# Kernel tuning notes

Measured on AMD Instinct MI355X. Metric: run time of the kernel, lower is better.

Reference implementation:

```python
import jax, jax.numpy as jnp
import numpy as np

B, T, C = 4, 2048, 1024
HEAD = 64  # n_embd // n_heads


def setup_inputs() -> dict:
    key = jax.random.key(0)
    kx, kk, kq, kv = jax.random.split(key, 4)
    x = jax.random.normal(kx, (B, T, C), dtype=jnp.float32)
    # nn.Linear(n_embd, head_size, bias=False) weights have shape [head_size, n_embd]
    s = 1.0 / np.sqrt(C)
    Wk = jax.random.normal(kk, (HEAD, C), dtype=jnp.float32) * s
    Wq = jax.random.normal(kq, (HEAD, C), dtype=jnp.float32) * s
    Wv = jax.random.normal(kv, (HEAD, C), dtype=jnp.float32) * s
    return {"x": x, "Wk": Wk, "Wq": Wq, "Wv": Wv}


def reference(x, Wk, Wq, Wv):
    Bx, Tx, Cx = x.shape
    k = jnp.einsum("btc,hc->bth", x, Wk)  # [B,T,HEAD]
    q = jnp.einsum("btc,hc->bth", x, Wq)
    v = jnp.einsum("btc,hc->bth", x, Wv)
    # NOTE: original scales by C**-0.5 (C = n_embd), not head_size**-0.5
    scale = Cx ** (-0.5)
    wei = jnp.einsum("bth,bsh->bts", q, k) * scale  # [B,T,T]
    causal = jnp.tril(jnp.ones((Tx, Tx), dtype=bool))
    wei = jnp.where(causal, wei, -jnp.inf)
    wei = jax.nn.softmax(wei, axis=-1)
    # dropout p=0.0 (eval) -> identity
    out = jnp.einsum("bts,bsh->bth", wei, v)  # [B,T,HEAD]
    return out
```

## Files before the change

### kernel.cpp

```cpp
#include <hip/hip_runtime.h>
#include <math.h>

#define Tn 2048
#define Cn 1024
#define Hn 64

using u16 = unsigned short;
using u32 = unsigned int;
typedef float f32x4 __attribute__((ext_vector_type(4)));
typedef __bf16 bf16x8 __attribute__((ext_vector_type(8)));
typedef u16 u16x8 __attribute__((ext_vector_type(8)));
typedef u32 u32x4 __attribute__((ext_vector_type(4)));

__device__ __forceinline__ u16 f2bf(float f) {
    return __builtin_bit_cast(u16, static_cast<__bf16>(f));
}

__global__ __launch_bounds__(256) void wpack_kernel(
    const float* __restrict__ Wk, const float* __restrict__ Wq,
    const float* __restrict__ Wv, u16* __restrict__ wp)
{
    int slot = blockIdx.x * 256 + threadIdx.x;
    int n16  = slot >> 11;
    int rem  = slot & 2047;
    int kc   = rem >> 6;
    int lane = rem & 63;
    int l15 = lane & 15, lg = lane >> 4;
    int col = n16 * 16 + l15;
    const float* __restrict__ Wm = (col < 64) ? Wk : (col < 128) ? Wq : Wv;
    float sc = (col >= 64 && col < 128) ? 0.03125f : 1.0f;
    const float* src = &Wm[(size_t)(col & 63) * Cn + kc * 32 + lg * 8];
    float4 lo = *reinterpret_cast<const float4*>(src);
    float4 hi = *reinterpret_cast<const float4*>(src + 4);
    u16x8 o;
    o[0] = f2bf(lo.x * sc); o[1] = f2bf(lo.y * sc);
    o[2] = f2bf(lo.z * sc); o[3] = f2bf(lo.w * sc);
    o[4] = f2bf(hi.x * sc); o[5] = f2bf(hi.y * sc);
    o[6] = f2bf(hi.z * sc); o[7] = f2bf(hi.w * sc);
    *reinterpret_cast<u16x8*>(&wp[(size_t)slot * 8]) = o;
}

__global__ __launch_bounds__(256) void qkv_proj(
    const float* __restrict__ x, const u16* __restrict__ wp,
    u16* __restrict__ kb, u16* __restrict__ qb, u16* __restrict__ vb)
{
    __shared__ float xs[2][32 * 68];

    const int tid  = threadIdx.x;
    const int lane = tid & 63;
    const int w    = tid >> 6;
    const int rg   = w & 1;
    const int cg   = w >> 1;
    const int l15  = lane & 15;
    const int lg   = lane >> 4;

    const int row0 = blockIdx.x * 32;
    const int sr   = tid >> 4;
    const int scc  = (tid & 15) << 2;

    f32x4 acc[6];
#pragma unroll
    for (int nt = 0; nt < 6; ++nt)
#pragma unroll
        for (int r = 0; r < 4; ++r) acc[nt][r] = 0.f;

    const float* __restrict__ xsrc0 = &x[(size_t)(row0 + sr) * Cn + scc];
    const float* __restrict__ xsrc1 = &x[(size_t)(row0 + sr + 16) * Cn + scc];
    const u16* __restrict__ wbase = wp + (size_t)cg * 6 * 32 * 64 * 8;

    float4 ga = *reinterpret_cast<const float4*>(xsrc0);
    float4 gb = *reinterpret_cast<const float4*>(xsrc1);
    *reinterpret_cast<float4*>(&xs[0][sr * 68 + scc]) = ga;
    *reinterpret_cast<float4*>(&xs[0][(sr + 16) * 68 + scc]) = gb;
    __syncthreads();

    for (int ks = 0; ks < 16; ++ks) {
        const int cur = ks & 1;
        if (ks < 15) {
            ga = *reinterpret_cast<const float4*>(xsrc0 + (ks + 1) * 64);
            gb = *reinterpret_cast<const float4*>(xsrc1 + (ks + 1) * 64);
        }
#pragma unroll
        for (int kc2 = 0; kc2 < 2; ++kc2) {
            const float* ap = &xs[cur][(rg * 16 + l15) * 68 + kc2 * 32 + (lg << 3)];
            f32x4 a0 = *reinterpret_cast<const f32x4*>(ap);
            f32x4 a1 = *reinterpret_cast<const f32x4*>(ap + 4);
            bf16x8 a;
            a[0] = (__bf16)a0[0]; a[1] = (__bf16)a0[1];
            a[2] = (__bf16)a0[2]; a[3] = (__bf16)a0[3];
            a[4] = (__bf16)a1[0]; a[5] = (__bf16)a1[1];
            a[6] = (__bf16)a1[2]; a[7] = (__bf16)a1[3];
            const int kcg = ks * 2 + kc2;
#pragma unroll
            for (int nt = 0; nt < 6; ++nt) {
                bf16x8 bfr = *reinterpret_cast<const bf16x8*>(
                    &wbase[(size_t)((nt * 32 + kcg) * 64 + lane) * 8]);
                acc[nt] = __builtin_amdgcn_mfma_f32_16x16x32_bf16(a, bfr, acc[nt], 0, 0, 0);
            }
        }
        if (ks < 15) {
            *reinterpret_cast<float4*>(&xs[cur ^ 1][sr * 68 + scc]) = ga;
            *reinterpret_cast<float4*>(&xs[cur ^ 1][(sr + 16) * 68 + scc]) = gb;
        }
        __syncthreads();
    }

#pragma unroll
    for (int nt = 0; nt < 6; ++nt) {
        const int col0 = cg * 96 + nt * 16;
        const int mat  = col0 >> 6;
        u16* __restrict__ ob = (mat == 0) ? kb : (mat == 1) ? qb : vb;
        const int h = (col0 & 63) + l15;
#pragma unroll
        for (int reg = 0; reg < 4; ++reg) {
            const int grow = row0 + rg * 16 + (lg << 2) + reg;
            ob[(size_t)grow * Hn + h] = f2bf(acc[nt][reg]);
        }
    }
}

__global__ __launch_bounds__(256) void attn(
    const u16* __restrict__ qb, const u16* __restrict__ kb,
    const u16* __restrict__ vb, float* __restrict__ Opart,
    float* __restrict__ mlb, float* __restrict__ out)
{
    __shared__ u16 Ks[2][64 * 72];
    __shared__ u16 VTs[2][64 * 72];

    const int tid  = threadIdx.x;
    const int lane = tid & 63;
    const int w    = tid >> 6;
    const int g    = w >> 1;
    const int p    = w & 1;
    const int l15  = lane & 15;
    const int lg   = lane >> 4;

    const int bid = blockIdx.x;
    const int b = bid / 160;
    const int r = bid % 160;
    int gq = 3;
    while (8 * gq * (gq + 1) > r) --gq;
    const int rr = r - 8 * gq * (gq + 1);
    const int qt = gq * 16 + rr / (gq + 1);
    const int c  = rr % (gq + 1);
    const int c8 = c * 8;

    const int t0  = qt * 32;
    const int wr0 = t0 + g * 16;
    const int nkt = (qt >> 1) + 1;
    const int rounds = (nkt - c8 + 1) >> 1 < 4 ? (nkt - c8 + 1) >> 1 : 4;
    const size_t kvbase = (size_t)b * Tn * Hn;

    bf16x8 qf[2];
    {
        const u16* qrow = qb + ((size_t)(b * Tn + wr0 + l15)) * Hn;
        qf[0] = *reinterpret_cast<const bf16x8*>(&qrow[(lg << 3)]);
        qf[1] = *reinterpret_cast<const bf16x8*>(&qrow[32 + (lg << 3)]);
    }

    f32x4 o[4];
    float m = -INFINITY, ls = 0.f;
#pragma unroll
    for (int nt = 0; nt < 4; ++nt)
#pragma unroll
        for (int rg2 = 0; rg2 < 4; ++rg2) o[nt][rg2] = 0.f;

    const int srcA = l15 + ((lane >> 4) & 1) * 32;
    const int srcB = srcA + 16;
    const bool hiSel = ((lg >> 1) & 1) != 0;

    for (int s = 0; s < rounds; ++s) {
        const int kt0 = c8 + 2 * s, kt1 = kt0 + 1;
        {
#pragma unroll
            for (int i = 0; i < 2; ++i) {
                int cc = tid + 256 * i;
                int rr2 = cc >> 3, cb = (cc & 7) << 3;
                *reinterpret_cast<u16x8*>(&Ks[0][rr2 * 72 + cb]) =
                    *reinterpret_cast<const u16x8*>(&kb[kvbase + (size_t)(kt0 * 64 + rr2) * Hn + cb]);
            }
#pragma unroll
            for (int i = 0; i < 2; ++i) {
                int cc = tid + 256 * i;
                int k = cc & 63, d0 = (cc >> 6) << 3;
                u16x8 v = *reinterpret_cast<const u16x8*>(&vb[kvbase + (size_t)(kt0 * 64 + k) * Hn + d0]);
#pragma unroll
                for (int j = 0; j < 8; ++j) VTs[0][(d0 + j) * 72 + k] = v[j];
            }
        }
        if (kt1 < nkt) {
#pragma unroll
            for (int i = 0; i < 2; ++i) {
                int cc = tid + 256 * i;
                int rr2 = cc >> 3, cb = (cc & 7) << 3;
                *reinterpret_cast<u16x8*>(&Ks[1][rr2 * 72 + cb]) =
                    *reinterpret_cast<const u16x8*>(&kb[kvbase + (size_t)(kt1 * 64 + rr2) * Hn + cb]);
            }
#pragma unroll
            for (int i = 0; i < 2; ++i) {
                int cc = tid + 256 * i;
                int k = cc & 63, d0 = (cc >> 6) << 3;
                u16x8 v = *reinterpret_cast<const u16x8*>(&vb[kvbase + (size_t)(kt1 * 64 + k) * Hn + d0]);
#pragma unroll
                for (int j = 0; j < 8; ++j) VTs[1][(d0 + j) * 72 + k] = v[j];
            }
        }
        __syncthreads();

        const int mykt = kt0 + p;
        if (mykt < nkt) {
            f32x4 sf[4];
#pragma unroll
            for (int nt = 0; nt < 4; ++nt)
#pragma unroll
                for (int rg2 = 0; rg2 < 4; ++rg2) sf[nt][rg2] = 0.f;
#pragma unroll
            for (int kc = 0; kc < 2; ++kc) {
#pragma unroll
                for (int nt = 0; nt < 4; ++nt) {
                    bf16x8 kf = *reinterpret_cast<const bf16x8*>(
                        &Ks[p][(nt * 16 + l15) * 72 + kc * 32 + (lg << 3)]);
                    sf[nt] = __builtin_amdgcn_mfma_f32_16x16x32_bf16(kf, qf[kc], sf[nt], 0, 0, 0);
                }
            }
            if (mykt * 64 + 63 > wr0) {
                const int tq = wr0 + l15;
#pragma unroll
                for (int nt = 0; nt < 4; ++nt) {
#pragma unroll
                    for (int reg = 0; reg < 4; ++reg) {
                        int kg = mykt * 64 + nt * 16 + (lg << 2) + reg;
                        if (kg > tq) sf[nt][reg] = -INFINITY;
                    }
                }
            }
            float tm = sf[0][0];
#pragma unroll
            for (int nt = 0; nt < 4; ++nt)
#pragma unroll
                for (int reg = 0; reg < 4; ++reg) tm = fmaxf(tm, sf[nt][reg]);
            tm = fmaxf(tm, __shfl_xor(tm, 16, 64));
            tm = fmaxf(tm, __shfl_xor(tm, 32, 64));
            if (!__all((tm <= m + 8.f) ? 1 : 0)) {
                float nm = fmaxf(m, tm);
                float al = __expf(m - nm);
                ls *= al;
                float alo[4];
#pragma unroll
                for (int reg = 0; reg < 4; ++reg)
                    alo[reg] = __shfl(al, (lg << 2) | reg, 64);
#pragma unroll
                for (int nt = 0; nt < 4; ++nt)
#pragma unroll
                    for (int reg = 0; reg < 4; ++reg) o[nt][reg] *= alo[reg];
                m = nm;
            }
            float pvv[4][4];
            float rs = 0.f;
#pragma unroll
            for (int nt = 0; nt < 4; ++nt)
#pragma unroll
                for (int reg = 0; reg < 4; ++reg) {
                    pvv[nt][reg] = __expf(sf[nt][reg] - m);
                    rs += pvv[nt][reg];
                }
            rs += __shfl_xor(rs, 16, 64);
            rs += __shfl_xor(rs, 32, 64);
            ls += rs;
            u32 wv[4][2];
#pragma unroll
            for (int nt = 0; nt < 4; ++nt)
#pragma unroll
                for (int h = 0; h < 2; ++h)
                    wv[nt][h] = (u32)f2bf(pvv[nt][2 * h]) |
                                ((u32)f2bf(pvv[nt][2 * h + 1]) << 16);
            bf16x8 pa[2];
#pragma unroll
            for (int kc = 0; kc < 2; ++kc) {
                u32 a0 = __shfl(wv[kc * 2][0], srcA, 64);
                u32 b0 = __shfl(wv[kc * 2 + 1][0], srcA, 64);
                u32 a1 = __shfl(wv[kc * 2][1], srcA, 64);
                u32 b1 = __shfl(wv[kc * 2 + 1][1], srcA, 64);
                u32 a2 = __shfl(wv[kc * 2][0], srcB, 64);
                u32 b2 = __shfl(wv[kc * 2 + 1][0], srcB, 64);
                u32 a3 = __shfl(wv[kc * 2][1], srcB, 64);
                u32 b3 = __shfl(wv[kc * 2 + 1][1], srcB, 64);
                u32x4 pw;
                pw[0] = hiSel ? b0 : a0;
                pw[1] = hiSel ? b1 : a1;
                pw[2] = hiSel ? b2 : a2;
                pw[3] = hiSel ? b3 : a3;
                pa[kc] = __builtin_bit_cast(bf16x8, pw);
            }
#pragma unroll
            for (int kc = 0; kc < 2; ++kc) {
#pragma unroll
                for (int nt = 0; nt < 4; ++nt) {
                    bf16x8 vf = *reinterpret_cast<const bf16x8*>(
                        &VTs[p][(nt * 16 + l15) * 72 + kc * 32 + (lg << 3)]);
                    o[nt] = __builtin_amdgcn_mfma_f32_16x16x32_bf16(pa[kc], vf, o[nt], 0, 0, 0);
                }
            }
        }
        __syncthreads();
    }

    float* slab = reinterpret_cast<float*>(&Ks[0][0]);
    float* sb = slab + g * (24 * 64);
    if (p == 1) {
#pragma unroll
        for (int nt = 0; nt < 4; ++nt)
#pragma unroll
            for (int reg = 0; reg < 4; ++reg)
                sb[(nt * 4 + reg) * 64 + lane] = o[nt][reg];
        if (lane < 16) {
            sb[1024 + lane] = m;
            sb[1040 + lane] = ls;
        }
    }
    __syncthreads();
    if (p == 0) {
        float mA[4], lA[4], mB[4], lB[4];
#pragma unroll
        for (int reg = 0; reg < 4; ++reg) {
            int q = (lg << 2) | reg;
            mA[reg] = __shfl(m, q, 64);
            lA[reg] = __shfl(ls, q, 64);
            mB[reg] = sb[1024 + q];
            lB[reg] = sb[1040 + q];
        }
        if (gq == 0) {
#pragma unroll
            for (int reg = 0; reg < 4; ++reg) {
                float ms = fmaxf(mA[reg], mB[reg]);
                float aA = __expf(mA[reg] - ms);
                float aB = __expf(mB[reg] - ms);
                float inv = 1.0f / (aA * lA[reg] + aB * lB[reg]);
                int grow = t0 + g * 16 + (lg << 2) + reg;
                float* orow = out + ((size_t)(b * Tn) + grow) * Hn;
#pragma unroll
                for (int nt = 0; nt < 4; ++nt)
                    orow[nt * 16 + l15] =
                        (aA * o[nt][reg] + aB * sb[(nt * 4 + reg) * 64 + lane]) * inv;
            }
        } else {
            const size_t pidx = (size_t)(b * 64 + qt) * 4 + c;
            float* __restrict__ ob = Opart + pidx * 2048;
#pragma unroll
            for (int reg = 0; reg < 4; ++reg) {
                float ms = fmaxf(mA[reg], mB[reg]);
                float aA = __expf(mA[reg] - ms);
                float aB = __expf(mB[reg] - ms);
                int row32 = g * 16 + (lg << 2) + reg;
                if (l15 == 0) {
                    float* mlp = mlb + pidx * 64 + row32 * 2;
                    mlp[0] = ms;
                    mlp[1] = aA * lA[reg] + aB * lB[reg];
                }
#pragma unroll
                for (int nt = 0; nt < 4; ++nt)
                    ob[row32 * 64 + nt * 16 + l15] =
                        aA * o[nt][reg] + aB * sb[(nt * 4 + reg) * 64 + lane];
            }
        }
    }
}

__global__ __launch_bounds__(256) void attn_merge(
    const float* __restrict__ Opart, const float* __restrict__ mlb,
    float* __restrict__ out)
{
    const int bid = blockIdx.x;
    const int b  = bid / 48;
    const int qt = 16 + bid % 48;
    const int nch = (qt >> 4) + 1;
    const int t = threadIdx.x;
    const int row = t >> 3, d0 = (t & 7) << 3;
    const size_t pbase = (size_t)(b * 64 + qt) * 4;

    float mc[4], lc[4];
#pragma unroll
    for (int cc = 0; cc < 4; ++cc) {
        if (cc < nch) {
            const float* mlp = mlb + (pbase + cc) * 64 + row * 2;
            mc[cc] = mlp[0];
            lc[cc] = mlp[1];
        } else { mc[cc] = -INFINITY; lc[cc] = 0.f; }
    }
    float mfin = fmaxf(fmaxf(mc[0], mc[1]), fmaxf(mc[2], mc[3]));

    float wgt[4], l = 0.f;
#pragma unroll
    for (int cc = 0; cc < 4; ++cc) {
        wgt[cc] = (cc < nch) ? __expf(mc[cc] - mfin) : 0.f;
        l += lc[cc] * wgt[cc];
    }

    f32x4 O0 = {0.f, 0.f, 0.f, 0.f}, O1 = {0.f, 0.f, 0.f, 0.f};
#pragma unroll
    for (int cc = 0; cc < 4; ++cc) {
        if (cc < nch) {
            const float* op = Opart + (pbase + cc) * 2048 + row * 64 + d0;
            f32x4 c0 = *reinterpret_cast<const f32x4*>(op);
            f32x4 c1 = *reinterpret_cast<const f32x4*>(op + 4);
            O0 += c0 * wgt[cc];
            O1 += c1 * wgt[cc];
        }
    }
    float inv = 1.f / l;
    float* orow = out + ((size_t)(b * Tn + qt * 32 + row)) * Hn + d0;
    *reinterpret_cast<f32x4*>(orow)     = O0 * inv;
    *reinterpret_cast<f32x4*>(orow + 4) = O1 * inv;
}

extern "C" void kernel_launch(void* const* d_in, const int* in_sizes, int n_in,
                              void* d_out, int out_size, void* d_ws, size_t ws_size,
                              hipStream_t stream) {
    const float* x  = (const float*)d_in[0];
    const float* Wk = (const float*)d_in[1];
    const float* Wq = (const float*)d_in[2];
    const float* Wv = (const float*)d_in[3];
    float* out = (float*)d_out;

    const size_t rows = (size_t)4 * Tn;
    u16* kbuf = (u16*)d_ws;
    u16* qbuf = kbuf + rows * Hn;
    u16* vbuf = qbuf + rows * Hn;
    u16* wpk  = vbuf + rows * Hn;
    float* Opart = (float*)(wpk + 196608);
    float* mlb   = Opart + (size_t)256 * 4 * 2048;

    wpack_kernel<<<96, 256, 0, stream>>>(Wk, Wq, Wv, wpk);
    qkv_proj<<<256, 256, 0, stream>>>(x, wpk, kbuf, qbuf, vbuf);
    attn<<<640, 256, 0, stream>>>(qbuf, kbuf, vbuf, Opart, mlb, out);
    attn_merge<<<192, 256, 0, stream>>>(Opart, mlb, out);
}
```

Before: 43.04 us.

## Share K/V LDS tiles across two query tiles per 512-thread block

Each attention block now covers two adjacent 32-row query tiles with 8 waves instead of 4, and the tiles share the same key/value range. K and V tiles are loaded and transposed into shared memory once for both. This halves the global K/V loads and LDS transpose cost per query row. In exchange the grid shrinks from 640 to 320 blocks, which may lower occupancy and load balance across CUs.

```diff
diff --git a/kernel.cpp b/kernel.cpp
--- a/kernel.cpp
+++ b/kernel.cpp
@@ -119,35 +119,37 @@
     }
 }
 
-__global__ __launch_bounds__(256) void attn(
+__global__ __launch_bounds__(512) void attn(
     const u16* __restrict__ qb, const u16* __restrict__ kb,
     const u16* __restrict__ vb, float* __restrict__ Opart,
     float* __restrict__ mlb, float* __restrict__ out)
 {
-    __shared__ u16 Ks[2][64 * 72];
-    __shared__ u16 VTs[2][64 * 72];
+    __shared__ u16 sm[18432];
+    u16* Ks  = sm;
+    u16* VTs = sm + 9216;
 
     const int tid  = threadIdx.x;
     const int lane = tid & 63;
     const int w    = tid >> 6;
-    const int g    = w >> 1;
+    const int qh   = w >> 2;
+    const int g    = (w >> 1) & 1;
     const int p    = w & 1;
     const int l15  = lane & 15;
     const int lg   = lane >> 4;
 
     const int bid = blockIdx.x;
-    const int b = bid / 160;
-    const int r = bid % 160;
-    int gq = 3;
-    while (8 * gq * (gq + 1) > r) --gq;
-    const int rr = r - 8 * gq * (gq + 1);
-    const int qt = gq * 16 + rr / (gq + 1);
-    const int c  = rr % (gq + 1);
-    const int c8 = c * 8;
-
-    const int t0  = qt * 32;
-    const int wr0 = t0 + g * 16;
-    const int nkt = (qt >> 1) + 1;
+    const int b = bid / 80;
+    const int r = bid % 80;
+    int gq, qp, c;
+    if (r < 8)       { gq = 0; qp = r;                 c = 0;            }
+    else if (r < 24) { gq = 1; qp = 8 + (r - 8) / 2;   c = (r - 8) % 2;  }
+    else if (r < 48) { gq = 2; qp = 16 + (r - 24) / 3; c = (r - 24) % 3; }
+    else             { gq = 3; qp = 24 + (r - 48) / 4; c = (r - 48) % 4; }
+    const int qt  = 2 * qp + qh;
+    const int c8  = c * 8;
+
+    const int wr0 = qt * 32 + g * 16;
+    const int nkt = qp + 1;
     const int rounds = (nkt - c8 + 1) >> 1 < 4 ? (nkt - c8 + 1) >> 1 : 4;
     const size_t kvbase = (size_t)b * Tn * Hn;
 
@@ -169,41 +171,24 @@
     const int srcB = srcA + 16;
     const bool hiSel = ((lg >> 1) & 1) != 0;
 
+    const int krow = tid >> 3, kcb = (tid & 7) << 3;
+    const int vk = tid & 63, vd0 = (tid >> 6) << 3;
+
     for (int s = 0; s < rounds; ++s) {
         const int kt0 = c8 + 2 * s, kt1 = kt0 + 1;
         {
-#pragma unroll
-            for (int i = 0; i < 2; ++i) {
-                int cc = tid + 256 * i;
-                int rr2 = cc >> 3, cb = (cc & 7) << 3;
-                *reinterpret_cast<u16x8*>(&Ks[0][rr2 * 72 + cb]) =
-                    *reinterpret_cast<const u16x8*>(&kb[kvbase + (size_t)(kt0 * 64 + rr2) * Hn + cb]);
-            }
-#pragma unroll
-            for (int i = 0; i < 2; ++i) {
-                int cc = tid + 256 * i;
-                int k = cc & 63, d0 = (cc >> 6) << 3;
-                u16x8 v = *reinterpret_cast<const u16x8*>(&vb[kvbase + (size_t)(kt0 * 64 + k) * Hn + d0]);
-#pragma unroll
-                for (int j = 0; j < 8; ++j) VTs[0][(d0 + j) * 72 + k] = v[j];
-            }
+            *reinterpret_cast<u16x8*>(&Ks[0 * 4608 + krow * 72 + kcb]) =
+                *reinterpret_cast<const u16x8*>(&kb[kvbase + (size_t)(kt0 * 64 + krow) * Hn + kcb]);
+            u16x8 v = *reinterpret_cast<const u16x8*>(&vb[kvbase + (size_t)(kt0 * 64 + vk) * Hn + vd0]);
+#pragma unroll
+            for (int j = 0; j < 8; ++j) VTs[0 * 4608 + (vd0 + j) * 72 + vk] = v[j];
         }
         if (kt1 < nkt) {
-#pragma unroll
-            for (int i = 0; i < 2; ++i) {
-                int cc = tid + 256 * i;
-                int rr2 = cc >> 3, cb = (cc & 7) << 3;
-                *reinterpret_cast<u16x8*>(&Ks[1][rr2 * 72 + cb]) =
-                    *reinterpret_cast<const u16x8*>(&kb[kvbase + (size_t)(kt1 * 64 + rr2) * Hn + cb]);
-            }
-#pragma unroll
-            for (int i = 0; i < 2; ++i) {
-                int cc = tid + 256 * i;
-                int k = cc & 63, d0 = (cc >> 6) << 3;
-                u16x8 v = *reinterpret_cast<const u16x8*>(&vb[kvbase + (size_t)(kt1 * 64 + k) * Hn + d0]);
-#pragma unroll
-                for (int j = 0; j < 8; ++j) VTs[1][(d0 + j) * 72 + k] = v[j];
-            }
+            *reinterpret_cast<u16x8*>(&Ks[1 * 4608 + krow * 72 + kcb]) =
+                *reinterpret_cast<const u16x8*>(&kb[kvbase + (size_t)(kt1 * 64 + krow) * Hn + kcb]);
+            u16x8 v = *reinterpret_cast<const u16x8*>(&vb[kvbase + (size_t)(kt1 * 64 + vk) * Hn + vd0]);
+#pragma unroll
+            for (int j = 0; j < 8; ++j) VTs[1 * 4608 + (vd0 + j) * 72 + vk] = v[j];
         }
         __syncthreads();
 
@@ -219,7 +204,7 @@
 #pragma unroll
                 for (int nt = 0; nt < 4; ++nt) {
                     bf16x8 kf = *reinterpret_cast<const bf16x8*>(
-                        &Ks[p][(nt * 16 + l15) * 72 + kc * 32 + (lg << 3)]);
+                        &Ks[p * 4608 + (nt * 16 + l15) * 72 + kc * 32 + (lg << 3)]);
                     sf[nt] = __builtin_amdgcn_mfma_f32_16x16x32_bf16(kf, qf[kc], sf[nt], 0, 0, 0);
                 }
             }
@@ -297,7 +282,7 @@
 #pragma unroll
                 for (int nt = 0; nt < 4; ++nt) {
                     bf16x8 vf = *reinterpret_cast<const bf16x8*>(
-                        &VTs[p][(nt * 16 + l15) * 72 + kc * 32 + (lg << 3)]);
+                        &VTs[p * 4608 + (nt * 16 + l15) * 72 + kc * 32 + (lg << 3)]);
                     o[nt] = __builtin_amdgcn_mfma_f32_16x16x32_bf16(pa[kc], vf, o[nt], 0, 0, 0);
                 }
             }
@@ -305,8 +290,8 @@
         __syncthreads();
     }
 
-    float* slab = reinterpret_cast<float*>(&Ks[0][0]);
-    float* sb = slab + g * (24 * 64);
+    float* slab = reinterpret_cast<float*>(sm);
+    float* sb = slab + (qh * 2 + g) * (24 * 64);
     if (p == 1) {
 #pragma unroll
         for (int nt = 0; nt < 4; ++nt)
@@ -336,7 +321,7 @@
                 float aA = __expf(mA[reg] - ms);
                 float aB = __expf(mB[reg] - ms);
                 float inv = 1.0f / (aA * lA[reg] + aB * lB[reg]);
-                int grow = t0 + g * 16 + (lg << 2) + reg;
+                int grow = wr0 + (lg << 2) + reg;
                 float* orow = out + ((size_t)(b * Tn) + grow) * Hn;
 #pragma unroll
                 for (int nt = 0; nt < 4; ++nt)
@@ -432,6 +417,6 @@
 
     wpack_kernel<<<96, 256, 0, stream>>>(Wk, Wq, Wv, wpk);
     qkv_proj<<<256, 256, 0, stream>>>(x, wpk, kbuf, qbuf, vbuf);
-    attn<<<640, 256, 0, stream>>>(qbuf, kbuf, vbuf, Opart, mlb, out);
+    attn<<<320, 512, 0, stream>>>(qbuf, kbuf, vbuf, Opart, mlb, out);
     attn_merge<<<192, 256, 0, stream>>>(Opart, mlb, out);
 }
```

Result: no change. 43.65 us (+1.4%).
